# Performance work log

Hardware: AMD Instinct MI355X
Metric: run time of the kernel (lower is better)

Reference implementation:

```python
import jax, jax.numpy as jnp
import numpy as np

B, C = 2048, 512          # batch, channels
CHG = 16                  # coarse grid side (16x16 -> N=256)
FHG = 16                  # fine grid side (16x16 -> F=256)
N = CHG * CHG             # coarse_span.total
F = FHG * FHG             # fine_total
K = 4                     # top4 sample mode
LOG_F = float(np.log(F))


def _ln(x, g, b, eps=1e-5):
    m = jnp.mean(x, axis=-1, keepdims=True)
    v = jnp.var(x, axis=-1, keepdims=True)
    return (x - m) * jax.lax.rsqrt(v + eps) * g + b


def _mlp3(x, w1, b1, w2, b2, w3, b3):
    # linear_stack: Linear+gelu, Linear+gelu, Linear (dropout=0 / eval)
    h = jax.nn.gelu(x @ w1 + b1)
    h = jax.nn.gelu(h @ w2 + b2)
    return h @ w3 + b3


def setup_inputs() -> dict:
    key = jax.random.key(0)
    ks = jax.random.split(key, 10)
    s = 0.02
    return {
        'x': jax.random.normal(ks[0], (B, C), jnp.float32),
        'in_g': jnp.ones((C,), jnp.float32), 'in_b': jnp.zeros((C,), jnp.float32),
        'nop_w': jax.random.normal(ks[1], (C, 1), jnp.float32) * s,
        'nop_b': jnp.zeros((1,), jnp.float32),
        'c_w1': jax.random.normal(ks[2], (C, C), jnp.float32) * s,
        'c_b1': jnp.zeros((C,), jnp.float32),
        'c_w2': jax.random.normal(ks[3], (C, C), jnp.float32) * s,
        'c_b2': jnp.zeros((C,), jnp.float32),
        'c_w3': jax.random.normal(ks[4], (C, N), jnp.float32) * s,
        'c_b3': jnp.zeros((N,), jnp.float32),
        'emb': jax.random.normal(ks[5], (N, C), jnp.float32),
        'emb_g': jnp.ones((C,), jnp.float32), 'emb_b': jnp.zeros((C,), jnp.float32),
        'f_w1': jax.random.normal(ks[6], (2 * C, C), jnp.float32) * s,
        'f_b1': jnp.zeros((C,), jnp.float32),
        'f_w2': jax.random.normal(ks[7], (C, C), jnp.float32) * s,
        'f_b2': jnp.zeros((C,), jnp.float32),
        'f_w3': jax.random.normal(ks[8], (C, F), jnp.float32) * s,
        'f_b3': jnp.zeros((F,), jnp.float32),
    }


def reference(x, in_g, in_b, nop_w, nop_b, c_w1, c_b1, c_w2, c_b2, c_w3, c_b3,
              emb, emb_g, emb_b, f_w1, f_b1, f_w2, f_b2, f_w3, f_b3):
    xn = _ln(x, in_g, in_b)                                  # (B,C)
    no_op = xn @ nop_w + nop_b                               # (B,1)
    coarse = _mlp3(xn, c_w1, c_b1, c_w2, c_b2, c_w3, c_b3)   # (B,N)
    _, idx = jax.lax.top_k(coarse, K)                        # (B,K) int32
    e = _ln(emb[idx], emb_g, emb_b)                          # (B,K,C)
    fin = jnp.concatenate([jnp.broadcast_to(xn[:, None, :], (B, K, C)), e], axis=-1)
    fine = _mlp3(fin, f_w1, f_b1, f_w2, f_b2, f_w3, f_b3)    # (B,K,F)
    # scatter value: coarse[b,i] - log F + fine + log F - lse(fine) = coarse[b,i] + log_softmax(fine)
    vals = jnp.take_along_axis(coarse, idx, axis=1)[:, :, None] + jax.nn.log_softmax(fine, axis=-1)
    dense = jnp.broadcast_to((coarse - LOG_F)[:, :, None], (B, N, F))
    dense = dense.at[jnp.arange(B)[:, None], idx].set(vals)  # top-k indices are distinct
    # view (B, ch0, ch1, fh0, fh1) -> permute (0,1,3,2,4) -> flatten
    xname = dense.reshape(B, CHG, CHG, FHG, FHG).transpose(0, 1, 3, 2, 4).reshape(B, -1)
    return jnp.concatenate([no_op, xname], axis=-1)          # (B, 1 + N*F)
```

## Files before the change

kernel.cpp:

```cpp
#include <hip/hip_runtime.h>
#include <math.h>

#define BATCH 2048
#define CH 512
#define N_COARSE 256
#define F_FINE 256
#define K_TOP 4
#define OUT_STRIDE 65537

typedef unsigned short ushort_t;
typedef __bf16 bf16x8 __attribute__((ext_vector_type(8)));
typedef float f32x4 __attribute__((ext_vector_type(4)));

__device__ __forceinline__ float gelu_tanh(float x) {
    float x3 = x * x * x;
    float t = tanhf(0.7978845608028654f * (x + 0.044715f * x3));
    return 0.5f * x * (1.0f + t);
}

__device__ __forceinline__ ushort_t f2bf(float f) {
    unsigned u = __float_as_uint(f);
    unsigned r = (u + 0x7FFF + ((u >> 16) & 1)) >> 16;
    return (ushort_t)r;
}

__global__ __launch_bounds__(256) void ln_noop_kernel(
    const float* __restrict__ x, const float* __restrict__ g, const float* __restrict__ b,
    const float* __restrict__ nop_w, const float* __restrict__ nop_b,
    float* __restrict__ xn, ushort_t* __restrict__ xn_bf, float* __restrict__ out)
{
    int row = blockIdx.x;
    int t = threadIdx.x;
    int lane = t & 63, wave = t >> 6;
    const float* xr = x + (size_t)row * CH;
    float v0 = xr[t], v1 = xr[t + 256];
    float s = v0 + v1, ss = v0 * v0 + v1 * v1;
    #pragma unroll
    for (int off = 32; off; off >>= 1) { s += __shfl_xor(s, off); ss += __shfl_xor(ss, off); }
    __shared__ float red[8];
    if (lane == 0) { red[wave] = s; red[4 + wave] = ss; }
    __syncthreads();
    s = red[0] + red[1] + red[2] + red[3];
    ss = red[4] + red[5] + red[6] + red[7];
    float mean = s * (1.0f / CH);
    float var = ss * (1.0f / CH) - mean * mean;
    float rsq = rsqrtf(var + 1e-5f);
    float xn0 = (v0 - mean) * rsq * g[t] + b[t];
    float xn1 = (v1 - mean) * rsq * g[t + 256] + b[t + 256];
    float* xnr = xn + (size_t)row * CH;
    xnr[t] = xn0; xnr[t + 256] = xn1;
    ushort_t* xbr = xn_bf + (size_t)row * CH;
    xbr[t] = f2bf(xn0); xbr[t + 256] = f2bf(xn1);
    float d = xn0 * nop_w[t] + xn1 * nop_w[t + 256];
    #pragma unroll
    for (int off = 32; off; off >>= 1) d += __shfl_xor(d, off);
    __syncthreads();
    if (lane == 0) red[wave] = d;
    __syncthreads();
    if (t == 0) out[(size_t)row * OUT_STRIDE] = red[0] + red[1] + red[2] + red[3] + nop_b[0];
}

__global__ __launch_bounds__(256) void convT_all_kernel(
    const float* __restrict__ w1, const float* __restrict__ w2, const float* __restrict__ w3,
    ushort_t* __restrict__ t1, ushort_t* __restrict__ t2, ushort_t* __restrict__ t3)
{
    __shared__ float s[32][33];
    int blk = blockIdx.x;
    const float* W; ushort_t* Wt; int Kd, Nd, gx, gy;
    if (blk < 512)      { W = w1; Wt = t1; Kd = 1024; Nd = 512; gx = blk & 15; gy = blk >> 4; }
    else if (blk < 768) { W = w2; Wt = t2; Kd = 512;  Nd = 512; gx = (blk - 512) & 15; gy = (blk - 512) >> 4; }
    else                { W = w3; Wt = t3; Kd = 512;  Nd = 256; gx = (blk - 768) & 7;  gy = (blk - 768) >> 3; }
    int tx = threadIdx.x & 31, ty = threadIdx.x >> 5;
    int n0 = gx * 32, k0 = gy * 32;
    #pragma unroll
    for (int i = 0; i < 4; ++i) {
        int r = ty + i * 8;
        s[r][tx] = W[(size_t)(k0 + r) * Nd + n0 + tx];
    }
    __syncthreads();
    #pragma unroll
    for (int i = 0; i < 4; ++i) {
        int r = ty + i * 8;
        Wt[(size_t)(n0 + r) * Kd + k0 + tx] = f2bf(s[tx][r]);
    }
}

template<bool GELU>
__global__ __launch_bounds__(256) void gemm_kernel(
    const float* __restrict__ A, const float* __restrict__ W,
    const float* __restrict__ bias, float* __restrict__ Cmat, int Nd, int Kd)
{
    __shared__ float As[2][32][68];
    __shared__ float Ws[2][32][68];
    int t = threadIdx.x;
    int tx = t & 15, ty = t >> 4;
    int n0 = blockIdx.x * 64, m0 = blockIdx.y * 64;

    float4 aR[2], wR[2];
    float acc[4][4] = {};

    auto loadAB = [&](int k0) {
        #pragma unroll
        for (int i = 0; i < 2; ++i) {
            int c = i * 256 + t;
            aR[i] = *(const float4*)&A[(size_t)(m0 + (c >> 3)) * Kd + k0 + (c & 7) * 4];
        }
        #pragma unroll
        for (int i = 0; i < 2; ++i) {
            int c = i * 256 + t;
            wR[i] = *(const float4*)&W[(size_t)(k0 + (c >> 4)) * Nd + n0 + (c & 15) * 4];
        }
    };
    auto storeAB = [&](int p) {
        #pragma unroll
        for (int i = 0; i < 2; ++i) {
            int c = i * 256 + t, r = c >> 3, kq = (c & 7) * 4;
            As[p][kq + 0][r] = aR[i].x; As[p][kq + 1][r] = aR[i].y;
            As[p][kq + 2][r] = aR[i].z; As[p][kq + 3][r] = aR[i].w;
        }
        #pragma unroll
        for (int i = 0; i < 2; ++i) {
            int c = i * 256 + t;
            *(float4*)&Ws[p][c >> 4][(c & 15) * 4] = wR[i];
        }
    };

    loadAB(0);
    storeAB(0);
    int steps = Kd >> 5;
    int p = 0;
    for (int s = 0; s < steps; ++s) {
        __syncthreads();
        if (s + 1 < steps) loadAB((s + 1) * 32);
        #pragma unroll
        for (int kk = 0; kk < 32; ++kk) {
            float4 a = *(const float4*)&As[p][kk][ty * 4];
            float4 w = *(const float4*)&Ws[p][kk][tx * 4];
            acc[0][0] += a.x * w.x; acc[0][1] += a.x * w.y; acc[0][2] += a.x * w.z; acc[0][3] += a.x * w.w;
            acc[1][0] += a.y * w.x; acc[1][1] += a.y * w.y; acc[1][2] += a.y * w.z; acc[1][3] += a.y * w.w;
            acc[2][0] += a.z * w.x; acc[2][1] += a.z * w.y; acc[2][2] += a.z * w.z; acc[2][3] += a.z * w.w;
            acc[3][0] += a.w * w.x; acc[3][1] += a.w * w.y; acc[3][2] += a.w * w.z; acc[3][3] += a.w * w.w;
        }
        if (s + 1 < steps) storeAB(p ^ 1);
        p ^= 1;
    }

    #pragma unroll
    for (int i = 0; i < 4; ++i) {
        int gm = m0 + ty * 4 + i;
        int gn0 = n0 + tx * 4;
        float4 o;
        float* po = &o.x;
        #pragma unroll
        for (int j = 0; j < 4; ++j) {
            float v = acc[i][j] + bias[gn0 + j];
            if (GELU) v = gelu_tanh(v);
            po[j] = v;
        }
        *(float4*)&Cmat[(size_t)gm * Nd + gn0] = o;
    }
}

template<int MT, int NT, bool CONCAT, bool GELU, bool OUT_BF16>
__global__ __launch_bounds__(256) void mfma_gemm_kernel(
    const ushort_t* __restrict__ A1, const ushort_t* __restrict__ A2, int K1,
    const ushort_t* __restrict__ Wt, const float* __restrict__ bias,
    void* __restrict__ Cout, int Nd, int Ktot)
{
    constexpr int AI = MT * 4 / 256, BI = NT * 4 / 256;
    constexpr int FI = MT / 32, FJ = NT / 32;
    __shared__ ushort_t As[2][MT * 32];
    __shared__ ushort_t Bs[2][NT * 32];
    int t = threadIdx.x;
    int n0 = blockIdx.x * NT, m0 = blockIdx.y * MT;
    int wave = t >> 6, lane = t & 63;
    int wm = (wave & 1) * (MT / 2), wn = (wave >> 1) * (NT / 2);
    int lr = lane & 15, quad = lane >> 4;

    f32x4 acc[FI][FJ] = {};
    float4 aReg[AI], bReg[BI];

    auto loadAB = [&](int k0) {
        #pragma unroll
        for (int i = 0; i < AI; ++i) {
            int c = i * 256 + t, r = c >> 2, q = (c & 3) * 8;
            int gr = m0 + r;
            const ushort_t* ap;
            if (CONCAT) ap = (k0 < K1) ? A1 + (size_t)(gr >> 2) * K1 + k0 + q
                                       : A2 + (size_t)gr * (Ktot - K1) + (k0 - K1) + q;
            else        ap = A1 + (size_t)gr * Ktot + k0 + q;
            aReg[i] = *(const float4*)ap;
        }
        #pragma unroll
        for (int i = 0; i < BI; ++i) {
            int c = i * 256 + t, r = c >> 2, q = (c & 3) * 8;
            bReg[i] = *(const float4*)(Wt + (size_t)(n0 + r) * Ktot + k0 + q);
        }
    };
    auto storeAB = [&](int p) {
        #pragma unroll
        for (int i = 0; i < AI; ++i) { int c = i * 256 + t; *(float4*)&As[p][c * 8] = aReg[i]; }
        #pragma unroll
        for (int i = 0; i < BI; ++i) { int c = i * 256 + t; *(float4*)&Bs[p][c * 8] = bReg[i]; }
    };

    loadAB(0);
    storeAB(0);
    int steps = Ktot >> 5;
    int p = 0;
    for (int s = 0; s < steps; ++s) {
        __syncthreads();
        if (s + 1 < steps) loadAB((s + 1) * 32);
        bf16x8 af[FI], bfr[FJ];
        #pragma unroll
        for (int i = 0; i < FI; ++i)
            af[i] = *(const bf16x8*)&As[p][(wm + i * 16 + lr) * 32 + quad * 8];
        #pragma unroll
        for (int j = 0; j < FJ; ++j)
            bfr[j] = *(const bf16x8*)&Bs[p][(wn + j * 16 + lr) * 32 + quad * 8];
        #pragma unroll
        for (int i = 0; i < FI; ++i)
            #pragma unroll
            for (int j = 0; j < FJ; ++j)
                acc[i][j] = __builtin_amdgcn_mfma_f32_16x16x32_bf16(af[i], bfr[j], acc[i][j], 0, 0, 0);
        if (s + 1 < steps) storeAB(p ^ 1);
        p ^= 1;
    }

    #pragma unroll
    for (int j = 0; j < FJ; ++j) {
        int col = n0 + wn + j * 16 + lr;
        float bv = bias[col];
        #pragma unroll
        for (int i = 0; i < FI; ++i) {
            #pragma unroll
            for (int r = 0; r < 4; ++r) {
                int row = m0 + wm + i * 16 + quad * 4 + r;
                float val = acc[i][j][r] + bv;
                if (GELU) val = gelu_tanh(val);
                if (OUT_BF16)
                    ((ushort_t*)Cout)[(size_t)row * Nd + col] = f2bf(val);
                else
                    ((float*)Cout)[(size_t)row * Nd + col] = val;
            }
        }
    }
}

__global__ __launch_bounds__(256) void topk_embln_kernel(
    const float* __restrict__ coarse, const float* __restrict__ emb,
    const float* __restrict__ g, const float* __restrict__ b,
    int* __restrict__ idx, float* __restrict__ cvals, ushort_t* __restrict__ e_bf)
{
    int brow = blockIdx.x;
    int t = threadIdx.x;
    int wave = t >> 6, lane = t & 63;
    __shared__ int sidx[4];

    if (wave == 0) {
        const float* cr = coarse + (size_t)brow * N_COARSE;
        float v[4]; int id[4];
        #pragma unroll
        for (int j = 0; j < 4; ++j) { v[j] = cr[lane + 64 * j]; id[j] = lane + 64 * j; }
        #pragma unroll
        for (int r = 0; r < K_TOP; ++r) {
            float bv = v[0]; int bi = id[0];
            #pragma unroll
            for (int j = 1; j < 4; ++j)
                if (v[j] > bv || (v[j] == bv && id[j] < bi)) { bv = v[j]; bi = id[j]; }
            #pragma unroll
            for (int off = 32; off; off >>= 1) {
                float ov = __shfl_xor(bv, off); int oi = __shfl_xor(bi, off);
                if (ov > bv || (ov == bv && oi < bi)) { bv = ov; bi = oi; }
            }
            if ((bi & 63) == lane) v[bi >> 6] = -INFINITY;
            if (lane == 0) {
                sidx[r] = bi;
                idx[brow * K_TOP + r] = bi;
                cvals[brow * K_TOP + r] = bv;
            }
        }
    }
    __syncthreads();

    int n = sidx[wave];
    const float* er = emb + (size_t)n * CH + lane * 8;
    float4 u0 = *(const float4*)er;
    float4 u1 = *(const float4*)(er + 4);
    float s  = u0.x + u0.y + u0.z + u0.w + u1.x + u1.y + u1.z + u1.w;
    float ss = u0.x * u0.x + u0.y * u0.y + u0.z * u0.z + u0.w * u0.w
             + u1.x * u1.x + u1.y * u1.y + u1.z * u1.z + u1.w * u1.w;
    #pragma unroll
    for (int off = 32; off; off >>= 1) { s += __shfl_xor(s, off); ss += __shfl_xor(ss, off); }
    float mean = s * (1.0f / CH);
    float var = ss * (1.0f / CH) - mean * mean;
    float rsq = rsqrtf(var + 1e-5f);
    float4 g0 = *(const float4*)(g + lane * 8), g1 = *(const float4*)(g + lane * 8 + 4);
    float4 b0 = *(const float4*)(b + lane * 8), b1 = *(const float4*)(b + lane * 8 + 4);
    uint4 pk;
    pk.x = (unsigned)f2bf((u0.x - mean) * rsq * g0.x + b0.x) |
           ((unsigned)f2bf((u0.y - mean) * rsq * g0.y + b0.y) << 16);
    pk.y = (unsigned)f2bf((u0.z - mean) * rsq * g0.z + b0.z) |
           ((unsigned)f2bf((u0.w - mean) * rsq * g0.w + b0.w) << 16);
    pk.z = (unsigned)f2bf((u1.x - mean) * rsq * g1.x + b1.x) |
           ((unsigned)f2bf((u1.y - mean) * rsq * g1.y + b1.y) << 16);
    pk.w = (unsigned)f2bf((u1.z - mean) * rsq * g1.z + b1.z) |
           ((unsigned)f2bf((u1.w - mean) * rsq * g1.w + b1.w) << 16);
    *(uint4*)(e_bf + (size_t)(brow * K_TOP + wave) * CH + lane * 8) = pk;
}

__global__ __launch_bounds__(64) void logsm_kernel(
    float* __restrict__ fine, const float* __restrict__ cvals)
{
    int row = blockIdx.x;
    int lane = threadIdx.x;
    float* fr = fine + (size_t)row * F_FINE;
    float v[4];
    #pragma unroll
    for (int j = 0; j < 4; ++j) v[j] = fr[lane + 64 * j];
    float mx = fmaxf(fmaxf(v[0], v[1]), fmaxf(v[2], v[3]));
    #pragma unroll
    for (int off = 32; off; off >>= 1) mx = fmaxf(mx, __shfl_xor(mx, off));
    float se = 0.f;
    #pragma unroll
    for (int j = 0; j < 4; ++j) se += expf(v[j] - mx);
    #pragma unroll
    for (int off = 32; off; off >>= 1) se += __shfl_xor(se, off);
    float addc = cvals[row] - mx - logf(se);
    #pragma unroll
    for (int j = 0; j < 4; ++j) fr[lane + 64 * j] = v[j] + addc;
}

__global__ __launch_bounds__(256) void scatter_kernel(
    const float* __restrict__ coarse, const float* __restrict__ fine,
    const int* __restrict__ idx, float* __restrict__ out)
{
    const float LOG_F = 5.545177444479562f;
    int b = blockIdx.y;
    int o = (blockIdx.x * 256 + threadIdx.x) * 4;
    int c0 = o >> 12, f0 = (o >> 8) & 15, c1 = (o >> 4) & 15, f1 = o & 15;
    int n = c0 * 16 + c1;
    int f = f0 * 16 + f1;
    int i0 = idx[b * 4 + 0], i1 = idx[b * 4 + 1], i2 = idx[b * 4 + 2], i3 = idx[b * 4 + 3];
    int k = -1;
    if (n == i0) k = 0; else if (n == i1) k = 1; else if (n == i2) k = 2; else if (n == i3) k = 3;
    float r0, r1, r2, r3;
    if (k >= 0) {
        const float* fr = fine + ((size_t)(b * 4 + k)) * F_FINE + f;
        r0 = fr[0]; r1 = fr[1]; r2 = fr[2]; r3 = fr[3];
    } else {
        float base = coarse[(size_t)b * N_COARSE + n] - LOG_F;
        r0 = r1 = r2 = r3 = base;
    }
    size_t ob = (size_t)b * OUT_STRIDE + 1 + o;
    __builtin_nontemporal_store(r0, &out[ob + 0]);
    __builtin_nontemporal_store(r1, &out[ob + 1]);
    __builtin_nontemporal_store(r2, &out[ob + 2]);
    __builtin_nontemporal_store(r3, &out[ob + 3]);
}

extern "C" void kernel_launch(void* const* d_in, const int* in_sizes, int n_in,
                              void* d_out, int out_size, void* d_ws, size_t ws_size,
                              hipStream_t stream) {
    const float* x     = (const float*)d_in[0];
    const float* in_g  = (const float*)d_in[1];
    const float* in_b  = (const float*)d_in[2];
    const float* nop_w = (const float*)d_in[3];
    const float* nop_b = (const float*)d_in[4];
    const float* c_w1  = (const float*)d_in[5];
    const float* c_b1  = (const float*)d_in[6];
    const float* c_w2  = (const float*)d_in[7];
    const float* c_b2  = (const float*)d_in[8];
    const float* c_w3  = (const float*)d_in[9];
    const float* c_b3  = (const float*)d_in[10];
    const float* emb   = (const float*)d_in[11];
    const float* emb_g = (const float*)d_in[12];
    const float* emb_b = (const float*)d_in[13];
    const float* f_w1  = (const float*)d_in[14];
    const float* f_b1  = (const float*)d_in[15];
    const float* f_w2  = (const float*)d_in[16];
    const float* f_b2  = (const float*)d_in[17];
    const float* f_w3  = (const float*)d_in[18];
    const float* f_b3  = (const float*)d_in[19];

    float* ws = (float*)d_ws;
    float* xn      = ws;
    float* h1      = xn + 1048576;
    float* h2      = h1 + 1048576;
    float* coarse  = h2 + 1048576;
    float* fine    = coarse + 524288;
    ushort_t* xn_bf  = (ushort_t*)(fine + 2097152);
    ushort_t* e_bf   = xn_bf + 1048576;
    ushort_t* fh1_bf = e_bf + 4194304;
    ushort_t* fh2_bf = fh1_bf + 4194304;
    ushort_t* wt1    = fh2_bf + 4194304;
    ushort_t* wt2    = wt1 + 524288;
    ushort_t* wt3    = wt2 + 262144;
    int*   idxb   = (int*)(wt3 + 131072);
    float* cvals  = (float*)(idxb + 8192);

    float* out = (float*)d_out;

    convT_all_kernel<<<896, 256, 0, stream>>>(f_w1, f_w2, f_w3, wt1, wt2, wt3);
    ln_noop_kernel<<<BATCH, 256, 0, stream>>>(x, in_g, in_b, nop_w, nop_b, xn, xn_bf, out);
    gemm_kernel<true><<<dim3(8, 32), 256, 0, stream>>>(xn, c_w1, c_b1, h1, 512, 512);
    gemm_kernel<true><<<dim3(8, 32), 256, 0, stream>>>(h1, c_w2, c_b2, h2, 512, 512);
    gemm_kernel<false><<<dim3(4, 32), 256, 0, stream>>>(h2, c_w3, c_b3, coarse, 256, 512);
    topk_embln_kernel<<<BATCH, 256, 0, stream>>>(coarse, emb, emb_g, emb_b, idxb, cvals, e_bf);
    mfma_gemm_kernel<128, 128, true, true, true><<<dim3(4, 64), 256, 0, stream>>>(
        xn_bf, e_bf, 512, wt1, f_b1, fh1_bf, 512, 1024);
    mfma_gemm_kernel<128, 128, false, true, true><<<dim3(4, 64), 256, 0, stream>>>(
        fh1_bf, nullptr, 0, wt2, f_b2, fh2_bf, 512, 512);
    mfma_gemm_kernel<64, 128, false, false, false><<<dim3(2, 128), 256, 0, stream>>>(
        fh2_bf, nullptr, 0, wt3, f_b3, fine, 256, 512);
    logsm_kernel<<<BATCH * K_TOP, 64, 0, stream>>>(fine, cvals);
    scatter_kernel<<<dim3(64, BATCH), 256, 0, stream>>>(coarse, fine, idxb, out);
}
```

Baseline: 800.4 us.

## Fuse prep kernels, log-softmax into GEMM epilogue; retile GEMMs and scatter

Result: faster. 777.4 us (-2.9%).

```diff
diff --git a/kernel.cpp b/kernel.cpp
--- a/kernel.cpp
+++ b/kernel.cpp
@@ -24,64 +24,63 @@
     return (ushort_t)r;
 }
 
-__global__ __launch_bounds__(256) void ln_noop_kernel(
+__global__ __launch_bounds__(256) void prep_kernel(
+    const float* __restrict__ w1, const float* __restrict__ w2, const float* __restrict__ w3,
+    ushort_t* __restrict__ t1, ushort_t* __restrict__ t2, ushort_t* __restrict__ t3,
     const float* __restrict__ x, const float* __restrict__ g, const float* __restrict__ b,
     const float* __restrict__ nop_w, const float* __restrict__ nop_b,
     float* __restrict__ xn, ushort_t* __restrict__ xn_bf, float* __restrict__ out)
 {
-    int row = blockIdx.x;
+    int blk = blockIdx.x;
     int t = threadIdx.x;
-    int lane = t & 63, wave = t >> 6;
-    const float* xr = x + (size_t)row * CH;
-    float v0 = xr[t], v1 = xr[t + 256];
-    float s = v0 + v1, ss = v0 * v0 + v1 * v1;
-    #pragma unroll
-    for (int off = 32; off; off >>= 1) { s += __shfl_xor(s, off); ss += __shfl_xor(ss, off); }
-    __shared__ float red[8];
-    if (lane == 0) { red[wave] = s; red[4 + wave] = ss; }
-    __syncthreads();
-    s = red[0] + red[1] + red[2] + red[3];
-    ss = red[4] + red[5] + red[6] + red[7];
-    float mean = s * (1.0f / CH);
-    float var = ss * (1.0f / CH) - mean * mean;
-    float rsq = rsqrtf(var + 1e-5f);
-    float xn0 = (v0 - mean) * rsq * g[t] + b[t];
-    float xn1 = (v1 - mean) * rsq * g[t + 256] + b[t + 256];
-    float* xnr = xn + (size_t)row * CH;
-    xnr[t] = xn0; xnr[t + 256] = xn1;
-    ushort_t* xbr = xn_bf + (size_t)row * CH;
-    xbr[t] = f2bf(xn0); xbr[t + 256] = f2bf(xn1);
-    float d = xn0 * nop_w[t] + xn1 * nop_w[t + 256];
-    #pragma unroll
-    for (int off = 32; off; off >>= 1) d += __shfl_xor(d, off);
-    __syncthreads();
-    if (lane == 0) red[wave] = d;
-    __syncthreads();
-    if (t == 0) out[(size_t)row * OUT_STRIDE] = red[0] + red[1] + red[2] + red[3] + nop_b[0];
-}
-
-__global__ __launch_bounds__(256) void convT_all_kernel(
-    const float* __restrict__ w1, const float* __restrict__ w2, const float* __restrict__ w3,
-    ushort_t* __restrict__ t1, ushort_t* __restrict__ t2, ushort_t* __restrict__ t3)
-{
-    __shared__ float s[32][33];
-    int blk = blockIdx.x;
-    const float* W; ushort_t* Wt; int Kd, Nd, gx, gy;
-    if (blk < 512)      { W = w1; Wt = t1; Kd = 1024; Nd = 512; gx = blk & 15; gy = blk >> 4; }
-    else if (blk < 768) { W = w2; Wt = t2; Kd = 512;  Nd = 512; gx = (blk - 512) & 15; gy = (blk - 512) >> 4; }
-    else                { W = w3; Wt = t3; Kd = 512;  Nd = 256; gx = (blk - 768) & 7;  gy = (blk - 768) >> 3; }
-    int tx = threadIdx.x & 31, ty = threadIdx.x >> 5;
-    int n0 = gx * 32, k0 = gy * 32;
-    #pragma unroll
-    for (int i = 0; i < 4; ++i) {
-        int r = ty + i * 8;
-        s[r][tx] = W[(size_t)(k0 + r) * Nd + n0 + tx];
-    }
-    __syncthreads();
-    #pragma unroll
-    for (int i = 0; i < 4; ++i) {
-        int r = ty + i * 8;
-        Wt[(size_t)(n0 + r) * Kd + k0 + tx] = f2bf(s[tx][r]);
+    if (blk < 896) {
+        __shared__ float s[32][33];
+        const float* W; ushort_t* Wt; int Kd, Nd, gx, gy;
+        if (blk < 512)      { W = w1; Wt = t1; Kd = 1024; Nd = 512; gx = blk & 15; gy = blk >> 4; }
+        else if (blk < 768) { W = w2; Wt = t2; Kd = 512;  Nd = 512; gx = (blk - 512) & 15; gy = (blk - 512) >> 4; }
+        else                { W = w3; Wt = t3; Kd = 512;  Nd = 256; gx = (blk - 768) & 7;  gy = (blk - 768) >> 3; }
+        int tx = t & 31, ty = t >> 5;
+        int n0 = gx * 32, k0 = gy * 32;
+        #pragma unroll
+        for (int i = 0; i < 4; ++i) {
+            int r = ty + i * 8;
+            s[r][tx] = W[(size_t)(k0 + r) * Nd + n0 + tx];
+        }
+        __syncthreads();
+        #pragma unroll
+        for (int i = 0; i < 4; ++i) {
+            int r = ty + i * 8;
+            Wt[(size_t)(n0 + r) * Kd + k0 + tx] = f2bf(s[tx][r]);
+        }
+    } else {
+        int row = blk - 896;
+        int lane = t & 63, wave = t >> 6;
+        const float* xr = x + (size_t)row * CH;
+        float v0 = xr[t], v1 = xr[t + 256];
+        float s = v0 + v1, ss = v0 * v0 + v1 * v1;
+        #pragma unroll
+        for (int off = 32; off; off >>= 1) { s += __shfl_xor(s, off); ss += __shfl_xor(ss, off); }
+        __shared__ float red[8];
+        if (lane == 0) { red[wave] = s; red[4 + wave] = ss; }
+        __syncthreads();
+        s = red[0] + red[1] + red[2] + red[3];
+        ss = red[4] + red[5] + red[6] + red[7];
+        float mean = s * (1.0f / CH);
+        float var = ss * (1.0f / CH) - mean * mean;
+        float rsq = rsqrtf(var + 1e-5f);
+        float xn0 = (v0 - mean) * rsq * g[t] + b[t];
+        float xn1 = (v1 - mean) * rsq * g[t + 256] + b[t + 256];
+        float* xnr = xn + (size_t)row * CH;
+        xnr[t] = xn0; xnr[t + 256] = xn1;
+        ushort_t* xbr = xn_bf + (size_t)row * CH;
+        xbr[t] = f2bf(xn0); xbr[t + 256] = f2bf(xn1);
+        float d = xn0 * nop_w[t] + xn1 * nop_w[t + 256];
+        #pragma unroll
+        for (int off = 32; off; off >>= 1) d += __shfl_xor(d, off);
+        __syncthreads();
+        if (lane == 0) red[wave] = d;
+        __syncthreads();
+        if (t == 0) out[(size_t)row * OUT_STRIDE] = red[0] + red[1] + red[2] + red[3] + nop_b[0];
     }
 }
 
@@ -91,13 +90,13 @@
     const float* __restrict__ bias, float* __restrict__ Cmat, int Nd, int Kd)
 {
     __shared__ float As[2][32][68];
-    __shared__ float Ws[2][32][68];
+    __shared__ float Ws[2][32][36];
     int t = threadIdx.x;
-    int tx = t & 15, ty = t >> 4;
-    int n0 = blockIdx.x * 64, m0 = blockIdx.y * 64;
-
-    float4 aR[2], wR[2];
-    float acc[4][4] = {};
+    int tx = t & 7, ty = t >> 3;
+    int n0 = blockIdx.x * 32, m0 = blockIdx.y * 64;
+
+    float4 aR[2]; float4 wR;
+    float acc[2][4] = {};
 
     auto loadAB = [&](int k0) {
         #pragma unroll
@@ -105,11 +104,7 @@
             int c = i * 256 + t;
             aR[i] = *(const float4*)&A[(size_t)(m0 + (c >> 3)) * Kd + k0 + (c & 7) * 4];
         }
-        #pragma unroll
-        for (int i = 0; i < 2; ++i) {
-            int c = i * 256 + t;
-            wR[i] = *(const float4*)&W[(size_t)(k0 + (c >> 4)) * Nd + n0 + (c & 15) * 4];
-        }
+        wR = *(const float4*)&W[(size_t)(k0 + (t >> 3)) * Nd + n0 + (t & 7) * 4];
     };
     auto storeAB = [&](int p) {
         #pragma unroll
@@ -118,11 +113,7 @@
             As[p][kq + 0][r] = aR[i].x; As[p][kq + 1][r] = aR[i].y;
             As[p][kq + 2][r] = aR[i].z; As[p][kq + 3][r] = aR[i].w;
         }
-        #pragma unroll
-        for (int i = 0; i < 2; ++i) {
-            int c = i * 256 + t;
-            *(float4*)&Ws[p][c >> 4][(c & 15) * 4] = wR[i];
-        }
+        *(float4*)&Ws[p][t >> 3][(t & 7) * 4] = wR;
     };
 
     loadAB(0);
@@ -134,20 +125,18 @@
         if (s + 1 < steps) loadAB((s + 1) * 32);
         #pragma unroll
         for (int kk = 0; kk < 32; ++kk) {
-            float4 a = *(const float4*)&As[p][kk][ty * 4];
+            float2 a = *(const float2*)&As[p][kk][ty * 2];
             float4 w = *(const float4*)&Ws[p][kk][tx * 4];
             acc[0][0] += a.x * w.x; acc[0][1] += a.x * w.y; acc[0][2] += a.x * w.z; acc[0][3] += a.x * w.w;
             acc[1][0] += a.y * w.x; acc[1][1] += a.y * w.y; acc[1][2] += a.y * w.z; acc[1][3] += a.y * w.w;
-            acc[2][0] += a.z * w.x; acc[2][1] += a.z * w.y; acc[2][2] += a.z * w.z; acc[2][3] += a.z * w.w;
-            acc[3][0] += a.w * w.x; acc[3][1] += a.w * w.y; acc[3][2] += a.w * w.z; acc[3][3] += a.w * w.w;
         }
         if (s + 1 < steps) storeAB(p ^ 1);
         p ^= 1;
     }
 
     #pragma unroll
-    for (int i = 0; i < 4; ++i) {
-        int gm = m0 + ty * 4 + i;
+    for (int i = 0; i < 2; ++i) {
+        int gm = m0 + ty * 2 + i;
         int gn0 = n0 + tx * 4;
         float4 o;
         float* po = &o.x;
@@ -161,16 +150,18 @@
     }
 }
 
-template<int MT, int NT, bool CONCAT, bool GELU, bool OUT_BF16>
+template<int MT, int NT, bool CONCAT, bool GELU, bool OUT_BF16, bool LOGSM>
 __global__ __launch_bounds__(256) void mfma_gemm_kernel(
     const ushort_t* __restrict__ A1, const ushort_t* __restrict__ A2, int K1,
     const ushort_t* __restrict__ Wt, const float* __restrict__ bias,
-    void* __restrict__ Cout, int Nd, int Ktot)
+    const float* __restrict__ cvals, void* __restrict__ Cout, int Nd, int Ktot)
 {
-    constexpr int AI = MT * 4 / 256, BI = NT * 4 / 256;
+    constexpr int AI = MT / 64, BI = NT / 64;
     constexpr int FI = MT / 32, FJ = NT / 32;
     __shared__ ushort_t As[2][MT * 32];
     __shared__ ushort_t Bs[2][NT * 32];
+    __shared__ float mxs[64][2];
+    __shared__ float ses[64][2];
     int t = threadIdx.x;
     int n0 = blockIdx.x * NT, m0 = blockIdx.y * MT;
     int wave = t >> 6, lane = t & 63;
@@ -227,21 +218,72 @@
         p ^= 1;
     }
 
-    #pragma unroll
-    for (int j = 0; j < FJ; ++j) {
-        int col = n0 + wn + j * 16 + lr;
-        float bv = bias[col];
-        #pragma unroll
-        for (int i = 0; i < FI; ++i) {
+    if (LOGSM) {
+        float bv[FJ];
+        #pragma unroll
+        for (int j = 0; j < FJ; ++j) bv[j] = bias[wn + j * 16 + lr];
+        int half = wave >> 1;
+        float rmx[FI][4];
+        #pragma unroll
+        for (int i = 0; i < FI; ++i)
             #pragma unroll
             for (int r = 0; r < 4; ++r) {
-                int row = m0 + wm + i * 16 + quad * 4 + r;
-                float val = acc[i][j][r] + bv;
-                if (GELU) val = gelu_tanh(val);
-                if (OUT_BF16)
-                    ((ushort_t*)Cout)[(size_t)row * Nd + col] = f2bf(val);
-                else
-                    ((float*)Cout)[(size_t)row * Nd + col] = val;
+                float m = -1e30f;
+                #pragma unroll
+                for (int j = 0; j < FJ; ++j) m = fmaxf(m, acc[i][j][r] + bv[j]);
+                #pragma unroll
+                for (int mk = 1; mk < 16; mk <<= 1) m = fmaxf(m, __shfl_xor(m, mk));
+                if (lr == 0) mxs[wm + i * 16 + quad * 4 + r][half] = m;
+            }
+        __syncthreads();
+        #pragma unroll
+        for (int i = 0; i < FI; ++i)
+            #pragma unroll
+            for (int r = 0; r < 4; ++r) {
+                int rl = wm + i * 16 + quad * 4 + r;
+                rmx[i][r] = fmaxf(mxs[rl][0], mxs[rl][1]);
+            }
+        #pragma unroll
+        for (int i = 0; i < FI; ++i)
+            #pragma unroll
+            for (int r = 0; r < 4; ++r) {
+                float s = 0.f;
+                #pragma unroll
+                for (int j = 0; j < FJ; ++j) s += expf(acc[i][j][r] + bv[j] - rmx[i][r]);
+                #pragma unroll
+                for (int mk = 1; mk < 16; mk <<= 1) s += __shfl_xor(s, mk);
+                if (lr == 0) ses[wm + i * 16 + quad * 4 + r][half] = s;
+            }
+        __syncthreads();
+        float* outp = (float*)Cout;
+        #pragma unroll
+        for (int i = 0; i < FI; ++i)
+            #pragma unroll
+            for (int r = 0; r < 4; ++r) {
+                int rl = wm + i * 16 + quad * 4 + r;
+                float se = ses[rl][0] + ses[rl][1];
+                float addc = cvals[m0 + rl] - rmx[i][r] - logf(se);
+                #pragma unroll
+                for (int j = 0; j < FJ; ++j)
+                    outp[(size_t)(m0 + rl) * Nd + wn + j * 16 + lr] = acc[i][j][r] + bv[j] + addc;
+            }
+    } else {
+        #pragma unroll
+        for (int j = 0; j < FJ; ++j) {
+            int col = n0 + wn + j * 16 + lr;
+            float bvv = bias[col];
+            #pragma unroll
+            for (int i = 0; i < FI; ++i) {
+                #pragma unroll
+                for (int r = 0; r < 4; ++r) {
+                    int row = m0 + wm + i * 16 + quad * 4 + r;
+                    float val = acc[i][j][r] + bvv;
+                    if (GELU) val = gelu_tanh(val);
+                    if (OUT_BF16)
+                        ((ushort_t*)Cout)[(size_t)row * Nd + col] = f2bf(val);
+                    else
+                        ((float*)Cout)[(size_t)row * Nd + col] = val;
+                }
             }
         }
     }
@@ -309,54 +351,39 @@
     *(uint4*)(e_bf + (size_t)(brow * K_TOP + wave) * CH + lane * 8) = pk;
 }
 
-__global__ __launch_bounds__(64) void logsm_kernel(
-    float* __restrict__ fine, const float* __restrict__ cvals)
-{
-    int row = blockIdx.x;
-    int lane = threadIdx.x;
-    float* fr = fine + (size_t)row * F_FINE;
-    float v[4];
-    #pragma unroll
-    for (int j = 0; j < 4; ++j) v[j] = fr[lane + 64 * j];
-    float mx = fmaxf(fmaxf(v[0], v[1]), fmaxf(v[2], v[3]));
-    #pragma unroll
-    for (int off = 32; off; off >>= 1) mx = fmaxf(mx, __shfl_xor(mx, off));
-    float se = 0.f;
-    #pragma unroll
-    for (int j = 0; j < 4; ++j) se += expf(v[j] - mx);
-    #pragma unroll
-    for (int off = 32; off; off >>= 1) se += __shfl_xor(se, off);
-    float addc = cvals[row] - mx - logf(se);
-    #pragma unroll
-    for (int j = 0; j < 4; ++j) fr[lane + 64 * j] = v[j] + addc;
-}
-
 __global__ __launch_bounds__(256) void scatter_kernel(
     const float* __restrict__ coarse, const float* __restrict__ fine,
     const int* __restrict__ idx, float* __restrict__ out)
 {
     const float LOG_F = 5.545177444479562f;
     int b = blockIdx.y;
-    int o = (blockIdx.x * 256 + threadIdx.x) * 4;
-    int c0 = o >> 12, f0 = (o >> 8) & 15, c1 = (o >> 4) & 15, f1 = o & 15;
-    int n = c0 * 16 + c1;
-    int f = f0 * 16 + f1;
-    int i0 = idx[b * 4 + 0], i1 = idx[b * 4 + 1], i2 = idx[b * 4 + 2], i3 = idx[b * 4 + 3];
-    int k = -1;
-    if (n == i0) k = 0; else if (n == i1) k = 1; else if (n == i2) k = 2; else if (n == i3) k = 3;
-    float r0, r1, r2, r3;
-    if (k >= 0) {
-        const float* fr = fine + ((size_t)(b * 4 + k)) * F_FINE + f;
-        r0 = fr[0]; r1 = fr[1]; r2 = fr[2]; r3 = fr[3];
-    } else {
-        float base = coarse[(size_t)b * N_COARSE + n] - LOG_F;
-        r0 = r1 = r2 = r3 = base;
-    }
-    size_t ob = (size_t)b * OUT_STRIDE + 1 + o;
-    __builtin_nontemporal_store(r0, &out[ob + 0]);
-    __builtin_nontemporal_store(r1, &out[ob + 1]);
-    __builtin_nontemporal_store(r2, &out[ob + 2]);
-    __builtin_nontemporal_store(r3, &out[ob + 3]);
+    __shared__ int sidx[4];
+    if (threadIdx.x < 4) sidx[threadIdx.x] = idx[b * 4 + threadIdx.x];
+    __syncthreads();
+    int i0 = sidx[0], i1 = sidx[1], i2 = sidx[2], i3 = sidx[3];
+    size_t rowb = (size_t)b * OUT_STRIDE + 1;
+    #pragma unroll
+    for (int q = 0; q < 4; ++q) {
+        int o = blockIdx.x * 4096 + q * 1024 + threadIdx.x * 4;
+        int c0 = o >> 12, f0 = (o >> 8) & 15, c1 = (o >> 4) & 15, f1 = o & 15;
+        int n = c0 * 16 + c1;
+        int f = f0 * 16 + f1;
+        int k = -1;
+        if (n == i0) k = 0; else if (n == i1) k = 1; else if (n == i2) k = 2; else if (n == i3) k = 3;
+        float r0, r1, r2, r3;
+        if (k >= 0) {
+            float4 u = *(const float4*)(fine + ((size_t)(b * 4 + k)) * F_FINE + f);
+            r0 = u.x; r1 = u.y; r2 = u.z; r3 = u.w;
+        } else {
+            float base = coarse[(size_t)b * N_COARSE + n] - LOG_F;
+            r0 = r1 = r2 = r3 = base;
+        }
+        float* p = out + rowb + o;
+        __builtin_nontemporal_store(r0, p + 0);
+        __builtin_nontemporal_store(r1, p + 1);
+        __builtin_nontemporal_store(r2, p + 2);
+        __builtin_nontemporal_store(r3, p + 3);
+    }
 }
 
 extern "C" void kernel_launch(void* const* d_in, const int* in_sizes, int n_in,
@@ -401,18 +428,18 @@
 
     float* out = (float*)d_out;
 
-    convT_all_kernel<<<896, 256, 0, stream>>>(f_w1, f_w2, f_w3, wt1, wt2, wt3);
-    ln_noop_kernel<<<BATCH, 256, 0, stream>>>(x, in_g, in_b, nop_w, nop_b, xn, xn_bf, out);
-    gemm_kernel<true><<<dim3(8, 32), 256, 0, stream>>>(xn, c_w1, c_b1, h1, 512, 512);
-    gemm_kernel<true><<<dim3(8, 32), 256, 0, stream>>>(h1, c_w2, c_b2, h2, 512, 512);
-    gemm_kernel<false><<<dim3(4, 32), 256, 0, stream>>>(h2, c_w3, c_b3, coarse, 256, 512);
+    prep_kernel<<<896 + BATCH, 256, 0, stream>>>(
+        f_w1, f_w2, f_w3, wt1, wt2, wt3,
+        x, in_g, in_b, nop_w, nop_b, xn, xn_bf, out);
+    gemm_kernel<true><<<dim3(16, 32), 256, 0, stream>>>(xn, c_w1, c_b1, h1, 512, 512);
+    gemm_kernel<true><<<dim3(16, 32), 256, 0, stream>>>(h1, c_w2, c_b2, h2, 512, 512);
+    gemm_kernel<false><<<dim3(8, 32), 256, 0, stream>>>(h2, c_w3, c_b3, coarse, 256, 512);
     topk_embln_kernel<<<BATCH, 256, 0, stream>>>(coarse, emb, emb_g, emb_b, idxb, cvals, e_bf);
-    mfma_gemm_kernel<128, 128, true, true, true><<<dim3(4, 64), 256, 0, stream>>>(
-        xn_bf, e_bf, 512, wt1, f_b1, fh1_bf, 512, 1024);
-    mfma_gemm_kernel<128, 128, false, true, true><<<dim3(4, 64), 256, 0, stream>>>(
-        fh1_bf, nullptr, 0, wt2, f_b2, fh2_bf, 512, 512);
-    mfma_gemm_kernel<64, 128, false, false, false><<<dim3(2, 128), 256, 0, stream>>>(
-        fh2_bf, nullptr, 0, wt3, f_b3, fine, 256, 512);
-    logsm_kernel<<<BATCH * K_TOP, 64, 0, stream>>>(fine, cvals);
-    scatter_kernel<<<dim3(64, BATCH), 256, 0, stream>>>(coarse, fine, idxb, out);
-}
+    mfma_gemm_kernel<64, 128, true, true, true, false><<<dim3(4, 128), 256, 0, stream>>>(
+        xn_bf, e_bf, 512, wt1, f_b1, nullptr, fh1_bf, 512, 1024);
+    mfma_gemm_kernel<64, 128, false, true, true, false><<<dim3(4, 128), 256, 0, stream>>>(
+        fh1_bf, nullptr, 0, wt2, f_b2, nullptr, fh2_bf, 512, 512);
+    mfma_gemm_kernel<64, 256, false, false, false, true><<<dim3(1, 128), 256, 0, stream>>>(
+        fh2_bf, nullptr, 0, wt3, f_b3, cvals, fine, 256, 512);
+    scatter_kernel<<<dim3(16, BATCH), 256, 0, stream>>>(coarse, fine, idxb, out);
+}
```
